# Performance work log

Measured on AMD Instinct MI355X. Metric: run time of the kernel, lower is better.

## Reference

```python
import jax, jax.numpy as jnp
import numpy as np

D_MODEL = 1024
NUM_HEADS = 16
D_K = D_MODEL // NUM_HEADS


def setup_inputs() -> dict:
    key = jax.random.key(0)
    ks = jax.random.split(key, 9)
    s = 1.0 / np.sqrt(D_MODEL)
    x = jax.random.normal(ks[0], (4, 2048, D_MODEL), dtype=jnp.float32)
    wq = jax.random.uniform(ks[1], (D_MODEL, D_MODEL), jnp.float32, -s, s)
    bq = jax.random.uniform(ks[2], (D_MODEL,), jnp.float32, -s, s)
    wk = jax.random.uniform(ks[3], (D_MODEL, D_MODEL), jnp.float32, -s, s)
    bk = jax.random.uniform(ks[4], (D_MODEL,), jnp.float32, -s, s)
    wv = jax.random.uniform(ks[5], (D_MODEL, D_MODEL), jnp.float32, -s, s)
    bv = jax.random.uniform(ks[6], (D_MODEL,), jnp.float32, -s, s)
    wo = jax.random.uniform(ks[7], (D_MODEL, D_MODEL), jnp.float32, -s, s)
    bo = jax.random.uniform(ks[8], (D_MODEL,), jnp.float32, -s, s)
    return {"x": x, "wq": wq, "bq": bq, "wk": wk, "bk": bk,
            "wv": wv, "bv": bv, "wo": wo, "bo": bo}


def reference(x, wq, bq, wk, bk, wv, bv, wo, bo):
    B, S, _ = x.shape
    H, Dk = NUM_HEADS, D_K
    # QKV projections (torch Linear: y = x @ W.T + b; here w* stored as [in,out])
    q = (x @ wq + bq).reshape(B, S, H, Dk).transpose(0, 2, 1, 3)  # [B,H,S,Dk]
    k = (x @ wk + bk).reshape(B, S, H, Dk).transpose(0, 2, 1, 3)
    v = (x @ wv + bv).reshape(B, S, H, Dk).transpose(0, 2, 1, 3)
    scores = jnp.einsum('bhqd,bhkd->bhqk', q, k) / jnp.sqrt(jnp.float32(Dk))
    attn = jax.nn.softmax(scores, axis=-1)
    out = jnp.einsum('bhqk,bhkd->bhqd', attn, v)  # [B,H,S,Dk]
    out = out.transpose(0, 2, 1, 3).reshape(B, S, H * Dk)
    return out @ wo + bo
```

## Files before the change

### kernel.cpp

```cpp
#include <hip/hip_runtime.h>
#include <hip/hip_bf16.h>
#include <cstdint>

#define D_MODEL 1024
#define NHEAD 16
#define DKH 64
#define BATCH 4
#define SEQ 2048
#define M_TOT (BATCH*SEQ)

typedef __bf16 bf16;
typedef __bf16 bf16x8 __attribute__((ext_vector_type(8)));
typedef __bf16 bf16x4 __attribute__((ext_vector_type(4)));
typedef float  f32x4  __attribute__((ext_vector_type(4)));
typedef float  f32x16 __attribute__((ext_vector_type(16)));

__device__ __forceinline__ void async_ld16(const void* g, void* l) {
    __builtin_amdgcn_global_load_lds(
        (__attribute__((address_space(1))) void*)(uintptr_t)g,
        (__attribute__((address_space(3))) void*)(uintptr_t)l,
        16, 0, 0);
}

__device__ __forceinline__ unsigned pack2_bf16(float lo, float hi) {
    union { __bf16 h[2]; unsigned u; } w;
    w.h[0] = (bf16)lo; w.h[1] = (bf16)hi;
    return w.u;
}

__global__ __launch_bounds__(256) void k_cvt(const float* __restrict__ x,
                                             bf16* __restrict__ xb,
                                             const float* __restrict__ wq,
                                             const float* __restrict__ wk,
                                             const float* __restrict__ wv,
                                             const float* __restrict__ wo,
                                             bf16* __restrict__ wt) {
    __shared__ float t[32][33];
    int bid = blockIdx.x;
    if (bid < 8192) {
        int i = (bid * 256 + threadIdx.x) * 4;
        float4 f = *(const float4*)(x + i);
        bf16x4 o;
        o[0] = (bf16)f.x; o[1] = (bf16)f.y; o[2] = (bf16)f.z; o[3] = (bf16)f.w;
        *(bf16x4*)(xb + i) = o;
    } else {
        int wb = bid - 8192;
        int z = wb >> 10;
        int rem = wb & 1023;
        const float* W = (z == 0) ? wq : (z == 1) ? wk : (z == 2) ? wv : wo;
        bf16* T = wt + (size_t)z * D_MODEL * D_MODEL;
        int tx = threadIdx.x & 31, ty = threadIdx.x >> 5;
        int bx = (rem & 31) * 32, by = (rem >> 5) * 32;
#pragma unroll
        for (int i = 0; i < 4; i++)
            t[ty + i * 8][tx] = W[(size_t)(by + ty + i * 8) * D_MODEL + bx + tx];
        __syncthreads();
#pragma unroll
        for (int i = 0; i < 4; i++)
            T[(size_t)(bx + ty + i * 8) * D_MODEL + by + tx] = (bf16)t[tx][ty + i * 8];
    }
}

__global__ __launch_bounds__(256) void k_gemm_qkv(const bf16* __restrict__ xb,
                                                  const bf16* __restrict__ wt,
                                                  const float* __restrict__ bq,
                                                  const float* __restrict__ bk,
                                                  const float* __restrict__ bv,
                                                  bf16* __restrict__ qkv,
                                                  bf16* __restrict__ vtg) {
    __shared__ bf16 As[2 * 128 * 32];
    __shared__ bf16 Bs[2 * 128 * 32];

    int tid = threadIdx.x;
    int lane = tid & 63, wid = tid >> 6;
    int ln = lane & 15, qd = lane >> 4;
    int wm = wid >> 1, wn = wid & 1;
    int m0 = blockIdx.x * 128;
    int n0 = blockIdx.y * 128;
    int z = n0 >> 10;
    const float* bias = (z == 0) ? bq : (z == 1) ? bk : bv;
    float scale = (z == 0) ? 0.125f * 1.44269504088896f : 1.0f;
    bool swapped = (z < 2);

    f32x4 zero4 = {0.f, 0.f, 0.f, 0.f};
    f32x4 acc[4][4];
#pragma unroll
    for (int i = 0; i < 4; i++)
#pragma unroll
        for (int j = 0; j < 4; j++) acc[i][j] = zero4;

    for (int k0 = 0; k0 < D_MODEL; k0 += 64) {
#pragma unroll
        for (int t = 0; t < 4; t++) {
            int c = t * 256 + tid;
            int ch = c >> 9, w = c & 511;
            int row = w >> 2, part = w & 3;
            async_ld16(xb + (size_t)(m0 + row) * D_MODEL + k0 + ch * 32 + part * 8,
                       As + ch * 4096 + (w & ~63) * 8);
            async_ld16(wt + (size_t)(n0 + row) * D_MODEL + k0 + ch * 32 + part * 8,
                       Bs + ch * 4096 + (w & ~63) * 8);
        }
        __syncthreads();
#pragma unroll
        for (int kc = 0; kc < 2; kc++) {
            bf16x8 af[4], bfr[4];
#pragma unroll
            for (int mi = 0; mi < 4; mi++)
                af[mi] = *(const bf16x8*)(As + kc * 4096 + (wm * 64 + mi * 16 + ln) * 32 + qd * 8);
#pragma unroll
            for (int ni = 0; ni < 4; ni++)
                bfr[ni] = *(const bf16x8*)(Bs + kc * 4096 + (wn * 64 + ni * 16 + ln) * 32 + qd * 8);
            if (swapped) {
#pragma unroll
                for (int mi = 0; mi < 4; mi++)
#pragma unroll
                    for (int ni = 0; ni < 4; ni++)
                        acc[mi][ni] = __builtin_amdgcn_mfma_f32_16x16x32_bf16(bfr[ni], af[mi],
                                                                              acc[mi][ni], 0, 0, 0);
            } else {
#pragma unroll
                for (int mi = 0; mi < 4; mi++)
#pragma unroll
                    for (int ni = 0; ni < 4; ni++)
                        acc[mi][ni] = __builtin_amdgcn_mfma_f32_16x16x32_bf16(af[mi], bfr[ni],
                                                                              acc[mi][ni], 0, 0, 0);
            }
        }
        __syncthreads();
    }

    if (swapped) {
        bf16* out = qkv + (size_t)z * M_TOT * D_MODEL;
#pragma unroll
        for (int mi = 0; mi < 4; mi++) {
            int srow = m0 + wm * 64 + mi * 16 + ln;
            int b = srow >> 11, s = srow & 2047;
#pragma unroll
            for (int ni = 0; ni < 4; ni++) {
                int colz = (n0 & 1023) + wn * 64 + ni * 16 + qd * 4;
                f32x4 bb = *(const f32x4*)(bias + colz);
                int h = colz >> 6, d = colz & 63;
                bf16x4 p;
#pragma unroll
                for (int r = 0; r < 4; r++)
                    p[r] = (bf16)((acc[mi][ni][r] + bb[r]) * scale);
                *(bf16x4*)(out + (((size_t)(b * NHEAD + h)) * SEQ + s) * DKH + d) = p;
            }
        }
    } else {
#pragma unroll
        for (int ni = 0; ni < 4; ni++) {
            int colz = (n0 & 1023) + wn * 64 + ni * 16 + ln;
            float bcol = bias[colz];
            int h = colz >> 6, d = colz & 63;
#pragma unroll
            for (int mi = 0; mi < 4; mi++) {
                int rb = m0 + wm * 64 + mi * 16 + qd * 4;
                int b = rb >> 11, s = rb & 2047;
                bf16x4 p;
#pragma unroll
                for (int r = 0; r < 4; r++)
                    p[r] = (bf16)(acc[mi][ni][r] + bcol);
                *(bf16x4*)(vtg + (((size_t)(b * NHEAD + h)) * DKH + d) * SEQ + s) = p;
            }
        }
    }
}

__global__ __launch_bounds__(256, 3) void k_attn(const bf16* __restrict__ qg,
                                                 const bf16* __restrict__ kg,
                                                 const bf16* __restrict__ vtg,
                                                 bf16* __restrict__ og) {
    __shared__ bf16 Ks[2 * 64 * 64];
    __shared__ bf16 Vs[2 * 64 * 64];

    int tid = threadIdx.x;
    int lane = tid & 63, wid = tid >> 6;
    int ln32 = lane & 31, hi = lane >> 5;
    int bh = blockIdx.x;
    int q0 = blockIdx.y * 128;
    int b = bh >> 4, h = bh & 15;

    const bf16* qp = qg + (size_t)bh * SEQ * DKH;
    const bf16* kp = kg + (size_t)bh * SEQ * DKH;
    const bf16* vp = vtg + (size_t)bh * DKH * SEQ;

    auto STAGE = [&](int bb, int kt) {
#pragma unroll
        for (int t = 0; t < 2; t++) {
            int c = t * 256 + tid;
            int row = c >> 3, chl = c & 7;
            int chg = chl ^ ((row ^ (row >> 3)) & 7);
            async_ld16(kp + (size_t)(kt + row) * DKH + chg * 8,
                       Ks + bb * 4096 + (c & ~63) * 8);
            async_ld16(vp + (size_t)row * SEQ + kt + chg * 8,
                       Vs + bb * 4096 + (c & ~63) * 8);
        }
    };

    STAGE(0, 0);

    bf16x8 qa[4];
#pragma unroll
    for (int kk = 0; kk < 4; kk++)
        qa[kk] = *(const bf16x8*)(qp + (size_t)(q0 + wid * 32 + ln32) * DKH + kk * 16 + hi * 8);

    f32x16 o_acc[2];
#pragma unroll
    for (int db = 0; db < 2; db++)
#pragma unroll
        for (int r = 0; r < 16; r++) o_acc[db][r] = 0.f;
    f32x4 lsum4 = {0.f, 0.f, 0.f, 0.f};

    asm volatile("s_waitcnt vmcnt(0)" ::: "memory");
    __builtin_amdgcn_s_barrier();

    for (int t = 0; t < 32; t++) {
        int bb = t & 1;
        if (t < 31) STAGE(bb ^ 1, (t + 1) * 64);

        f32x16 sc[2];
#pragma unroll
        for (int kb = 0; kb < 2; kb++)
#pragma unroll
            for (int r = 0; r < 16; r++) sc[kb][r] = 0.f;
#pragma unroll
        for (int kk = 0; kk < 4; kk++) {
#pragma unroll
            for (int kb = 0; kb < 2; kb++) {
                int kr = kb * 32 + ln32;
                bf16x8 kf = *(const bf16x8*)(Ks + bb * 4096 + kr * 64
                                + (size_t)(((2 * kk + hi) ^ ((kr ^ (kr >> 3)) & 7)) * 8));
                sc[kb] = __builtin_amdgcn_mfma_f32_32x32x16_bf16(kf, qa[kk], sc[kb], 0, 0, 0);
            }
        }

#pragma unroll
        for (int kb = 0; kb < 2; kb++) {
            float e[16];
#pragma unroll
            for (int r = 0; r < 16; r++) e[r] = __builtin_amdgcn_exp2f(sc[kb][r]);
#pragma unroll
            for (int r = 0; r < 16; r++) lsum4[r & 3] += e[r];
            unsigned pd[8];
#pragma unroll
            for (int j = 0; j < 8; j++) pd[j] = pack2_bf16(e[2 * j], e[2 * j + 1]);
#pragma unroll
            for (int ks = 0; ks < 2; ks++) {
                unsigned a0 = pd[ks * 4 + 0], b0 = pd[ks * 4 + 2];
                unsigned a1 = pd[ks * 4 + 1], b1 = pd[ks * 4 + 3];
                asm volatile("v_permlane32_swap_b32 %0, %1" : "+v"(a0), "+v"(b0));
                asm volatile("v_permlane32_swap_b32 %0, %1" : "+v"(a1), "+v"(b1));
                union { unsigned u[4]; bf16x8 v; } pf;
                pf.u[0] = a0; pf.u[1] = a1; pf.u[2] = b0; pf.u[3] = b1;
#pragma unroll
                for (int db = 0; db < 2; db++) {
                    int vr = db * 32 + ln32;
                    bf16x8 vf = *(const bf16x8*)(Vs + bb * 4096 + vr * 64
                                    + (size_t)(((4 * kb + 2 * ks + hi) ^ ((vr ^ (vr >> 3)) & 7)) * 8));
                    o_acc[db] = __builtin_amdgcn_mfma_f32_32x32x16_bf16(vf, pf.v, o_acc[db], 0, 0, 0);
                }
            }
        }

        if (t < 31) {
            asm volatile("s_waitcnt vmcnt(0)" ::: "memory");
            __builtin_amdgcn_s_barrier();
        }
    }

    float lsum = (lsum4[0] + lsum4[1]) + (lsum4[2] + lsum4[3]);
    float lt = lsum + __shfl_xor(lsum, 32, 64);
    float inv = 1.0f / lt;

    int s = q0 + wid * 32 + ln32;
    size_t rowoff = ((size_t)b * SEQ + s) * D_MODEL + h * DKH;
#pragma unroll
    for (int db = 0; db < 2; db++)
#pragma unroll
        for (int q4 = 0; q4 < 4; q4++) {
            bf16x4 pv4;
#pragma unroll
            for (int j = 0; j < 4; j++) pv4[j] = (bf16)(o_acc[db][q4 * 4 + j] * inv);
            *(bf16x4*)(og + rowoff + db * 32 + q4 * 8 + hi * 4) = pv4;
        }
}

__global__ __launch_bounds__(256) void k_gemm_out(const bf16* __restrict__ ob,
                                                  const bf16* __restrict__ wot,
                                                  const float* __restrict__ bo,
                                                  float* __restrict__ out) {
    __shared__ bf16 As[2 * 128 * 32];
    __shared__ bf16 Bs[2 * 128 * 32];

    int tid = threadIdx.x;
    int lane = tid & 63, wid = tid >> 6;
    int ln = lane & 15, qd = lane >> 4;
    int wm = wid >> 1, wn = wid & 1;
    int m0 = blockIdx.x * 128, n0 = blockIdx.y * 128;

    f32x4 zero4 = {0.f, 0.f, 0.f, 0.f};
    f32x4 acc[4][4];
#pragma unroll
    for (int i = 0; i < 4; i++)
#pragma unroll
        for (int j = 0; j < 4; j++) acc[i][j] = zero4;

    for (int k0 = 0; k0 < D_MODEL; k0 += 64) {
#pragma unroll
        for (int t = 0; t < 4; t++) {
            int c = t * 256 + tid;
            int ch = c >> 9, w = c & 511;
            int row = w >> 2, part = w & 3;
            async_ld16(ob + (size_t)(m0 + row) * D_MODEL + k0 + ch * 32 + part * 8,
                       As + ch * 4096 + (w & ~63) * 8);
            async_ld16(wot + (size_t)(n0 + row) * D_MODEL + k0 + ch * 32 + part * 8,
                       Bs + ch * 4096 + (w & ~63) * 8);
        }
        __syncthreads();
#pragma unroll
        for (int kc = 0; kc < 2; kc++) {
            bf16x8 af[4], bfr[4];
#pragma unroll
            for (int mi = 0; mi < 4; mi++)
                af[mi] = *(const bf16x8*)(As + kc * 4096 + (wm * 64 + mi * 16 + ln) * 32 + qd * 8);
#pragma unroll
            for (int ni = 0; ni < 4; ni++)
                bfr[ni] = *(const bf16x8*)(Bs + kc * 4096 + (wn * 64 + ni * 16 + ln) * 32 + qd * 8);
#pragma unroll
            for (int mi = 0; mi < 4; mi++)
#pragma unroll
                for (int ni = 0; ni < 4; ni++)
                    acc[mi][ni] = __builtin_amdgcn_mfma_f32_16x16x32_bf16(bfr[ni], af[mi],
                                                                          acc[mi][ni], 0, 0, 0);
        }
        __syncthreads();
    }

#pragma unroll
    for (int mi = 0; mi < 4; mi++) {
        int row = m0 + wm * 64 + mi * 16 + ln;
#pragma unroll
        for (int ni = 0; ni < 4; ni++) {
            int col4 = n0 + wn * 64 + ni * 16 + qd * 4;
            f32x4 bb = *(const f32x4*)(bo + col4);
            f32x4 v;
#pragma unroll
            for (int r = 0; r < 4; r++) v[r] = acc[mi][ni][r] + bb[r];
            *(f32x4*)(out + (size_t)row * D_MODEL + col4) = v;
        }
    }
}

extern "C" void kernel_launch(void* const* d_in, const int* in_sizes, int n_in,
                              void* d_out, int out_size, void* d_ws, size_t ws_size,
                              hipStream_t stream) {
    const float* x  = (const float*)d_in[0];
    const float* wq = (const float*)d_in[1];
    const float* bq = (const float*)d_in[2];
    const float* wk = (const float*)d_in[3];
    const float* bk = (const float*)d_in[4];
    const float* wv = (const float*)d_in[5];
    const float* bv = (const float*)d_in[6];
    const float* wo = (const float*)d_in[7];
    const float* bo = (const float*)d_in[8];
    float* out = (float*)d_out;

    char* ws = (char*)d_ws;
    bf16* xb  = (bf16*)ws;
    bf16* wt  = (bf16*)(ws + 16777216);
    bf16* qkv = (bf16*)(ws + 25165824);
    bf16* vtg = (bf16*)(ws + 75497472);
    bf16* og  = xb;

    k_cvt<<<dim3(8192 + 4096), dim3(256), 0, stream>>>(x, xb, wq, wk, wv, wo, wt);
    k_gemm_qkv<<<dim3(64, 24), dim3(256), 0, stream>>>(xb, wt, bq, bk, bv, qkv, vtg);
    k_attn<<<dim3(64, 16), dim3(256), 0, stream>>>(qkv, qkv + (size_t)M_TOT * D_MODEL, vtg, og);
    k_gemm_out<<<dim3(64, 8), dim3(256), 0, stream>>>(og, wt + 3 * (size_t)D_MODEL * D_MODEL,
                                                      bo, out);
}
```

Before: 290.8 us.

## Precompute LDS offsets, unroll attention loop by two, add MFMA priority hints

The attention kernel now computes global and LDS addresses once, before the loop, and holds them in registers. It also unrolls the KV loop by two so the double-buffer index is a compile-time constant, and wraps the MFMA bursts in s_setprio. The exp, row-sum and bf16-pack steps are fused into a single loop, and the launch_bounds occupancy hint of 3 is removed. The aim is to cut per-iteration address arithmetic and improve interleaving of matrix and vector work across waves. The cost is extra register pressure, and dropping the occupancy hint may lower occupancy.

```diff
diff --git a/kernel.cpp b/kernel.cpp
--- a/kernel.cpp
+++ b/kernel.cpp
@@ -167,10 +167,10 @@
     }
 }
 
-__global__ __launch_bounds__(256, 3) void k_attn(const bf16* __restrict__ qg,
-                                                 const bf16* __restrict__ kg,
-                                                 const bf16* __restrict__ vtg,
-                                                 bf16* __restrict__ og) {
+__global__ __launch_bounds__(256) void k_attn(const bf16* __restrict__ qg,
+                                              const bf16* __restrict__ kg,
+                                              const bf16* __restrict__ vtg,
+                                              bf16* __restrict__ og) {
     __shared__ bf16 Ks[2 * 64 * 64];
     __shared__ bf16 Vs[2 * 64 * 64];
 
@@ -185,20 +185,45 @@
     const bf16* kp = kg + (size_t)bh * SEQ * DKH;
     const bf16* vp = vtg + (size_t)bh * DKH * SEQ;
 
+    int cA = tid, cB = 256 + tid;
+    int rowA = cA >> 3, rowB = cB >> 3;
+    int chgA = (cA & 7) ^ ((rowA ^ (rowA >> 3)) & 7);
+    int chgB = (cB & 7) ^ ((rowB ^ (rowB >> 3)) & 7);
+    const bf16* kgA = kp + rowA * DKH + chgA * 8;
+    const bf16* kgB = kp + rowB * DKH + chgB * 8;
+    const bf16* vgA = vp + (size_t)rowA * SEQ + chgA * 8;
+    const bf16* vgB = vp + (size_t)rowB * SEQ + chgB * 8;
+    bf16* ldKA = Ks + (cA & ~63) * 8;
+    bf16* ldKB = Ks + (cB & ~63) * 8;
+    bf16* ldVA = Vs + (cA & ~63) * 8;
+    bf16* ldVB = Vs + (cB & ~63) * 8;
+
     auto STAGE = [&](int bb, int kt) {
-#pragma unroll
-        for (int t = 0; t < 2; t++) {
-            int c = t * 256 + tid;
-            int row = c >> 3, chl = c & 7;
-            int chg = chl ^ ((row ^ (row >> 3)) & 7);
-            async_ld16(kp + (size_t)(kt + row) * DKH + chg * 8,
-                       Ks + bb * 4096 + (c & ~63) * 8);
-            async_ld16(vp + (size_t)row * SEQ + kt + chg * 8,
-                       Vs + bb * 4096 + (c & ~63) * 8);
-        }
+        async_ld16(kgA + (size_t)kt * DKH, ldKA + bb * 4096);
+        async_ld16(vgA + kt,               ldVA + bb * 4096);
+        async_ld16(kgB + (size_t)kt * DKH, ldKB + bb * 4096);
+        async_ld16(vgB + kt,               ldVB + bb * 4096);
     };
 
     STAGE(0, 0);
+
+    unsigned koff[2][4], voff[2][4];
+#pragma unroll
+    for (int kb = 0; kb < 2; kb++) {
+        int kr = kb * 32 + ln32;
+        int sw = (kr ^ (kr >> 3)) & 7;
+#pragma unroll
+        for (int kk = 0; kk < 4; kk++)
+            koff[kb][kk] = (unsigned)((kr * 64 + (((2 * kk + hi) ^ sw) * 8)) * 2);
+    }
+#pragma unroll
+    for (int db = 0; db < 2; db++) {
+        int vr = db * 32 + ln32;
+        int sw = (vr ^ (vr >> 3)) & 7;
+#pragma unroll
+        for (int j = 0; j < 4; j++)
+            voff[db][j] = (unsigned)((vr * 64 + (((2 * j + hi) ^ sw) * 8)) * 2);
+    }
 
     bf16x8 qa[4];
 #pragma unroll
@@ -212,39 +237,42 @@
         for (int r = 0; r < 16; r++) o_acc[db][r] = 0.f;
     f32x4 lsum4 = {0.f, 0.f, 0.f, 0.f};
 
+    f32x16 z16;
+#pragma unroll
+    for (int r = 0; r < 16; r++) z16[r] = 0.f;
+
     asm volatile("s_waitcnt vmcnt(0)" ::: "memory");
     __builtin_amdgcn_s_barrier();
 
-    for (int t = 0; t < 32; t++) {
-        int bb = t & 1;
-        if (t < 31) STAGE(bb ^ 1, (t + 1) * 64);
+    auto TILE = [&](int bb) {
+        const char* Kb = (const char*)Ks + bb * 8192;
+        const char* Vb = (const char*)Vs + bb * 8192;
 
         f32x16 sc[2];
-#pragma unroll
-        for (int kb = 0; kb < 2; kb++)
-#pragma unroll
-            for (int r = 0; r < 16; r++) sc[kb][r] = 0.f;
-#pragma unroll
-        for (int kk = 0; kk < 4; kk++) {
-#pragma unroll
-            for (int kb = 0; kb < 2; kb++) {
-                int kr = kb * 32 + ln32;
-                bf16x8 kf = *(const bf16x8*)(Ks + bb * 4096 + kr * 64
-                                + (size_t)(((2 * kk + hi) ^ ((kr ^ (kr >> 3)) & 7)) * 8));
+        __builtin_amdgcn_s_setprio(1);
+#pragma unroll
+        for (int kb = 0; kb < 2; kb++) {
+            bf16x8 kf0 = *(const bf16x8*)(Kb + koff[kb][0]);
+            sc[kb] = __builtin_amdgcn_mfma_f32_32x32x16_bf16(kf0, qa[0], z16, 0, 0, 0);
+#pragma unroll
+            for (int kk = 1; kk < 4; kk++) {
+                bf16x8 kf = *(const bf16x8*)(Kb + koff[kb][kk]);
                 sc[kb] = __builtin_amdgcn_mfma_f32_32x32x16_bf16(kf, qa[kk], sc[kb], 0, 0, 0);
             }
         }
+        __builtin_amdgcn_s_setprio(0);
 
 #pragma unroll
         for (int kb = 0; kb < 2; kb++) {
-            float e[16];
-#pragma unroll
-            for (int r = 0; r < 16; r++) e[r] = __builtin_amdgcn_exp2f(sc[kb][r]);
-#pragma unroll
-            for (int r = 0; r < 16; r++) lsum4[r & 3] += e[r];
             unsigned pd[8];
 #pragma unroll
-            for (int j = 0; j < 8; j++) pd[j] = pack2_bf16(e[2 * j], e[2 * j + 1]);
+            for (int j = 0; j < 8; j++) {
+                float e0 = __builtin_amdgcn_exp2f(sc[kb][2 * j]);
+                float e1 = __builtin_amdgcn_exp2f(sc[kb][2 * j + 1]);
+                lsum4[2 * (j & 1)]     += e0;
+                lsum4[2 * (j & 1) + 1] += e1;
+                pd[j] = pack2_bf16(e0, e1);
+            }
 #pragma unroll
             for (int ks = 0; ks < 2; ks++) {
                 unsigned a0 = pd[ks * 4 + 0], b0 = pd[ks * 4 + 2];
@@ -253,17 +281,25 @@
                 asm volatile("v_permlane32_swap_b32 %0, %1" : "+v"(a1), "+v"(b1));
                 union { unsigned u[4]; bf16x8 v; } pf;
                 pf.u[0] = a0; pf.u[1] = a1; pf.u[2] = b0; pf.u[3] = b1;
+                __builtin_amdgcn_s_setprio(1);
 #pragma unroll
                 for (int db = 0; db < 2; db++) {
-                    int vr = db * 32 + ln32;
-                    bf16x8 vf = *(const bf16x8*)(Vs + bb * 4096 + vr * 64
-                                    + (size_t)(((4 * kb + 2 * ks + hi) ^ ((vr ^ (vr >> 3)) & 7)) * 8));
+                    bf16x8 vf = *(const bf16x8*)(Vb + voff[db][2 * kb + ks]);
                     o_acc[db] = __builtin_amdgcn_mfma_f32_32x32x16_bf16(vf, pf.v, o_acc[db], 0, 0, 0);
                 }
-            }
-        }
-
-        if (t < 31) {
+                __builtin_amdgcn_s_setprio(0);
+            }
+        }
+    };
+
+    for (int t = 0; t < 32; t += 2) {
+        STAGE(1, (t + 1) * 64);
+        TILE(0);
+        asm volatile("s_waitcnt vmcnt(0)" ::: "memory");
+        __builtin_amdgcn_s_barrier();
+        if (t < 30) STAGE(0, (t + 2) * 64);
+        TILE(1);
+        if (t < 30) {
             asm volatile("s_waitcnt vmcnt(0)" ::: "memory");
             __builtin_amdgcn_s_barrier();
         }
```

Result: no change. 294.3 us (+1.2%).
